# Optimization experiments

Hardware: AMD Instinct MI355X
Metric: run time of the kernel (lower is better)

## Reference

```python
import jax, jax.numpy as jnp
import numpy as np
from jax import lax

GAMMA = 2        # unused in forward (kept for fidelity to source)
PW = 10.0
THRESHOLD = 1.0
ERODE = 3
BACKZERO = 0

B, C, D, H, W = 2, 1, 128, 256, 256


def setup_inputs() -> dict:
    key = jax.random.key(0)
    k1, k2 = jax.random.split(key)
    inp = jax.random.normal(k1, (B, C, D, H, W), dtype=jnp.float32)
    tgt = jax.random.uniform(k2, (B, C, D, H, W), dtype=jnp.float32)
    return {"input": inp, "target": tgt}


def _box_sum_3d(x, r):
    # All-ones (2r+1)^3 conv3d with padding=r == sliding-window sum (shape-preserving).
    k = 2 * r + 1
    return lax.reduce_window(
        x, 0.0, lax.add,
        window_dimensions=(1, 1, k, k, k),
        window_strides=(1, 1, 1, 1, 1),
        padding=[(0, 0), (0, 0), (r, r), (r, r), (r, r)],
    )


def reference(input, target):
    # weight = clamp(target, 0, threshold); zero out voxels exactly at threshold
    w = jnp.clip(target, 0.0, THRESHOLD)
    w = w - THRESHOLD * (w == THRESHOLD).astype(jnp.float32)
    # box-filter "erosion" then binarize
    w = _box_sum_3d(w, ERODE)
    w = (w > 0).astype(jnp.float32)
    w = 1.0 + w * PW
    if BACKZERO != 0:
        mask = (input < 0).astype(jnp.float32) * (target == 0).astype(jnp.float32)
        w = w * (1.0 - mask)
    loss = jnp.abs(target - input) * w
    return jnp.mean(loss)
```

## Files before the change

### kernel.cpp

```cpp
#include <hip/hip_runtime.h>
#include <stdint.h>

#define BB 2
#define DD 128
#define HH 256
#define WW 256
static constexpr int64_t N = (int64_t)BB * DD * HH * WW;
static constexpr int WPR    = WW / 64;
static constexpr int NWORDS = BB * DD * HH * WPR;
static constexpr int NROWS  = BB * DD * HH;
static constexpr int K1_BLOCKS = NROWS / 8;
static constexpr int K2_BLOCKS = (HH / 16) * (DD / 16) * (BB * WPR);

__global__ __launch_bounds__(256) void mask_xdil_sum(const float* __restrict__ tgt,
                                                     const float* __restrict__ inp,
                                                     uint64_t* __restrict__ mask,
                                                     double* __restrict__ p0) {
    const int wave = threadIdx.x >> 6;
    const int lane = threadIdx.x & 63;
    float s = 0.0f;

    #pragma unroll
    for (int r = 0; r < 2; ++r) {
        const int row = blockIdx.x * 8 + wave * 2 + r;
        const int64_t base = (int64_t)row * WW;
        const float4 t = ((const float4*)(tgt + base))[lane];
        const float4 a = ((const float4*)(inp + base))[lane];

        s += fabsf(t.x - a.x) + fabsf(t.y - a.y)
           + fabsf(t.z - a.z) + fabsf(t.w - a.w);

        const uint64_t b0 = __ballot(t.x > 0.0f && t.x < 1.0f);
        const uint64_t b1 = __ballot(t.y > 0.0f && t.y < 1.0f);
        const uint64_t b2 = __ballot(t.z > 0.0f && t.z < 1.0f);
        const uint64_t b3 = __ballot(t.w > 0.0f && t.w < 1.0f);

        const uint64_t U  = b0 | b1 | b2 | b3;
        const uint64_t d0 = U | ((b1 | b2 | b3) << 1);
        const uint64_t d1 = U | ((b2 | b3) << 1) | (b0 >> 1);
        const uint64_t d2 = U | (b3 << 1) | ((b0 | b1) >> 1);
        const uint64_t d3 = U | ((b0 | b1 | b2) >> 1);

        const uint64_t dv = (lane & 2) ? ((lane & 1) ? d3 : d2)
                                       : ((lane & 1) ? d1 : d0);
        if (lane < 4)
            mask[(int64_t)row * WPR + lane] = dv;
    }

    #pragma unroll
    for (int off = 32; off > 0; off >>= 1)
        s += __shfl_down(s, off, 64);
    __shared__ float wsum[4];
    if (lane == 0) wsum[wave] = s;
    __syncthreads();
    if (threadIdx.x == 0)
        p0[blockIdx.x] = (double)((wsum[0] + wsum[1]) + (wsum[2] + wsum[3]));
}

__global__ __launch_bounds__(256) void yz_dil_reduce(const uint64_t* __restrict__ in,
                                                     const float* __restrict__ inp,
                                                     const float* __restrict__ tgt,
                                                     double* __restrict__ p1) {
    __shared__ uint64_t raw[22][23];
    __shared__ uint64_t yd[22][17];
    const int ty = threadIdx.x & 15;
    const int tz = threadIdx.x >> 4;
    const int y0 = blockIdx.x * 16;
    const int z0 = blockIdx.y * 16;
    const int b  = blockIdx.z >> 2;
    const int wx = blockIdx.z & 3;

    for (int idx = threadIdx.x; idx < 22 * 22; idx += 256) {
        const int zz = idx / 22, yy = idx % 22;
        const int gz = z0 - 3 + zz, gy = y0 - 3 + yy;
        uint64_t v = 0;
        if (gz >= 0 && gz < DD && gy >= 0 && gy < HH)
            v = in[(((int64_t)(b * DD + gz)) * HH + gy) * WPR + wx];
        raw[zz][yy] = v;
    }
    __syncthreads();

    for (int idx = threadIdx.x; idx < 22 * 16; idx += 256) {
        const int zz = idx >> 4, yy = idx & 15;
        uint64_t v = 0;
        #pragma unroll
        for (int d = 0; d < 7; d++) v |= raw[zz][yy + d];
        yd[zz][yy] = v;
    }
    __syncthreads();

    uint64_t v = 0;
    #pragma unroll
    for (int d = 0; d < 7; d++) v |= yd[tz + d][ty];

    float sab = 0.0f;
    if (v != ~0ull) {
        uint64_t z = ~v;
        const int64_t vox = (((int64_t)(b * DD + z0 + tz)) * HH + y0 + ty) * WW + wx;
        while (z) {
            const int l = __ffsll((unsigned long long)z) - 1;
            z &= z - 1;
            const int64_t o = vox + 4 * (int64_t)l;
            sab += fabsf(tgt[o] - inp[o]);
        }
    }

    #pragma unroll
    for (int off = 32; off > 0; off >>= 1)
        sab += __shfl_down(sab, off, 64);
    __shared__ float ws[4];
    const int lane = threadIdx.x & 63;
    const int wv   = threadIdx.x >> 6;
    if (lane == 0) ws[wv] = sab;
    __syncthreads();
    if (threadIdx.x == 0) {
        const int flat = blockIdx.x + gridDim.x * (blockIdx.y + gridDim.y * blockIdx.z);
        p1[flat] = (double)((ws[0] + ws[1]) + (ws[2] + ws[3]));
    }
}

__global__ __launch_bounds__(1024) void finalize(const double* __restrict__ p0,
                                                 const double* __restrict__ p1,
                                                 float* __restrict__ out) {
    double s0 = 0.0, sa = 0.0;
    for (int i = threadIdx.x; i < K1_BLOCKS; i += 1024) s0 += p0[i];
    for (int i = threadIdx.x; i < K2_BLOCKS; i += 1024) sa += p1[i];
    #pragma unroll
    for (int off = 32; off > 0; off >>= 1) {
        s0 += __shfl_down(s0, off, 64);
        sa += __shfl_down(sa, off, 64);
    }
    __shared__ double w0[16], wa[16];
    const int lane = threadIdx.x & 63;
    const int wv   = threadIdx.x >> 6;
    if (lane == 0) { w0[wv] = s0; wa[wv] = sa; }
    __syncthreads();
    if (threadIdx.x == 0) {
        double S0 = 0.0, SA = 0.0;
        #pragma unroll
        for (int k = 0; k < 16; k++) { S0 += w0[k]; SA += wa[k]; }
        out[0] = (float)((11.0 * S0 - 10.0 * SA) / (double)N);
    }
}

extern "C" void kernel_launch(void* const* d_in, const int* in_sizes, int n_in,
                              void* d_out, int out_size, void* d_ws, size_t ws_size,
                              hipStream_t stream) {
    const float* inp = (const float*)d_in[0];
    const float* tgt = (const float*)d_in[1];
    float* out = (float*)d_out;

    double*   p0    = (double*)d_ws;
    double*   p1    = (double*)((char*)d_ws + 96 * 1024);
    uint64_t* mask0 = (uint64_t*)((char*)d_ws + 256 * 1024);

    mask_xdil_sum<<<K1_BLOCKS, 256, 0, stream>>>(tgt, inp, mask0, p0);
    yz_dil_reduce<<<dim3(HH / 16, DD / 16, BB * WPR), 256, 0, stream>>>(mask0, inp, tgt, p1);
    finalize<<<1, 1024, 0, stream>>>(p0, p1, out);
}
```

Baseline: 149.4 us.

## Fuse final reduction into second kernel via atomics and batch row loads

The separate finalize launch is removed. Each block of the second kernel folds a slice of the first kernel's per-wave partials with its own partial sum, adds the result atomically to a global accumulator, and the last block (found with a ticket counter) writes the mean. The first kernel now uses a fixed grid of 2048 blocks. Each wave handles 8 strided rows and issues 4 rows of loads at a time to raise memory-level parallelism. This saves one launch and the tail reduction, at the cost of double atomics and a nondeterministic summation order.

Result: slower. 170.1 us (+13.9%).

```diff
diff --git a/kernel.cpp b/kernel.cpp
--- a/kernel.cpp
+++ b/kernel.cpp
@@ -7,60 +7,71 @@
 #define WW 256
 static constexpr int64_t N = (int64_t)BB * DD * HH * WW;
 static constexpr int WPR    = WW / 64;
-static constexpr int NWORDS = BB * DD * HH * WPR;
 static constexpr int NROWS  = BB * DD * HH;
-static constexpr int K1_BLOCKS = NROWS / 8;
+static constexpr int K1_BLOCKS = 2048;
+static constexpr int NWAVES = K1_BLOCKS * 4;
+static constexpr int ROWS_PER_WAVE = NROWS / NWAVES;
 static constexpr int K2_BLOCKS = (HH / 16) * (DD / 16) * (BB * WPR);
+static constexpr int P0_PER_K2 = NWAVES / K2_BLOCKS;
 
 __global__ __launch_bounds__(256) void mask_xdil_sum(const float* __restrict__ tgt,
                                                      const float* __restrict__ inp,
                                                      uint64_t* __restrict__ mask,
-                                                     double* __restrict__ p0) {
-    const int wave = threadIdx.x >> 6;
+                                                     double* __restrict__ p0,
+                                                     double* __restrict__ acc,
+                                                     unsigned* __restrict__ counter) {
     const int lane = threadIdx.x & 63;
+    const int wg   = (blockIdx.x << 2) | (threadIdx.x >> 6);
+
+    if (blockIdx.x == 0 && threadIdx.x == 0) { *acc = 0.0; *counter = 0u; }
+
     float s = 0.0f;
+    #pragma unroll
+    for (int h = 0; h < 2; ++h) {
+        float4 t[4], a[4];
+        #pragma unroll
+        for (int k = 0; k < 4; ++k) {
+            const int row = wg + (h * 4 + k) * NWAVES;
+            t[k] = ((const float4*)(tgt + (int64_t)row * WW))[lane];
+            a[k] = ((const float4*)(inp + (int64_t)row * WW))[lane];
+        }
+        #pragma unroll
+        for (int k = 0; k < 4; ++k) {
+            const int row = wg + (h * 4 + k) * NWAVES;
+            s += fabsf(t[k].x - a[k].x) + fabsf(t[k].y - a[k].y)
+               + fabsf(t[k].z - a[k].z) + fabsf(t[k].w - a[k].w);
 
-    #pragma unroll
-    for (int r = 0; r < 2; ++r) {
-        const int row = blockIdx.x * 8 + wave * 2 + r;
-        const int64_t base = (int64_t)row * WW;
-        const float4 t = ((const float4*)(tgt + base))[lane];
-        const float4 a = ((const float4*)(inp + base))[lane];
+            const uint64_t b0 = __ballot(t[k].x > 0.0f && t[k].x < 1.0f);
+            const uint64_t b1 = __ballot(t[k].y > 0.0f && t[k].y < 1.0f);
+            const uint64_t b2 = __ballot(t[k].z > 0.0f && t[k].z < 1.0f);
+            const uint64_t b3 = __ballot(t[k].w > 0.0f && t[k].w < 1.0f);
 
-        s += fabsf(t.x - a.x) + fabsf(t.y - a.y)
-           + fabsf(t.z - a.z) + fabsf(t.w - a.w);
+            const uint64_t U  = b0 | b1 | b2 | b3;
+            const uint64_t d0 = U | ((b1 | b2 | b3) << 1);
+            const uint64_t d1 = U | ((b2 | b3) << 1) | (b0 >> 1);
+            const uint64_t d2 = U | (b3 << 1) | ((b0 | b1) >> 1);
+            const uint64_t d3 = U | ((b0 | b1 | b2) >> 1);
 
-        const uint64_t b0 = __ballot(t.x > 0.0f && t.x < 1.0f);
-        const uint64_t b1 = __ballot(t.y > 0.0f && t.y < 1.0f);
-        const uint64_t b2 = __ballot(t.z > 0.0f && t.z < 1.0f);
-        const uint64_t b3 = __ballot(t.w > 0.0f && t.w < 1.0f);
-
-        const uint64_t U  = b0 | b1 | b2 | b3;
-        const uint64_t d0 = U | ((b1 | b2 | b3) << 1);
-        const uint64_t d1 = U | ((b2 | b3) << 1) | (b0 >> 1);
-        const uint64_t d2 = U | (b3 << 1) | ((b0 | b1) >> 1);
-        const uint64_t d3 = U | ((b0 | b1 | b2) >> 1);
-
-        const uint64_t dv = (lane & 2) ? ((lane & 1) ? d3 : d2)
-                                       : ((lane & 1) ? d1 : d0);
-        if (lane < 4)
-            mask[(int64_t)row * WPR + lane] = dv;
+            const uint64_t dv = (lane & 2) ? ((lane & 1) ? d3 : d2)
+                                           : ((lane & 1) ? d1 : d0);
+            if (lane < 4)
+                mask[(int64_t)row * WPR + lane] = dv;
+        }
     }
 
     #pragma unroll
     for (int off = 32; off > 0; off >>= 1)
         s += __shfl_down(s, off, 64);
-    __shared__ float wsum[4];
-    if (lane == 0) wsum[wave] = s;
-    __syncthreads();
-    if (threadIdx.x == 0)
-        p0[blockIdx.x] = (double)((wsum[0] + wsum[1]) + (wsum[2] + wsum[3]));
+    if (lane == 0) p0[wg] = (double)s;
 }
 
 __global__ __launch_bounds__(256) void yz_dil_reduce(const uint64_t* __restrict__ in,
                                                      const float* __restrict__ inp,
                                                      const float* __restrict__ tgt,
-                                                     double* __restrict__ p1) {
+                                                     const double* __restrict__ p0,
+                                                     double* __restrict__ acc,
+                                                     unsigned* __restrict__ counter,
+                                                     float* __restrict__ out) {
     __shared__ uint64_t raw[22][23];
     __shared__ uint64_t yd[22][17];
     const int ty = threadIdx.x & 15;
@@ -113,33 +124,20 @@
     const int wv   = threadIdx.x >> 6;
     if (lane == 0) ws[wv] = sab;
     __syncthreads();
+
     if (threadIdx.x == 0) {
         const int flat = blockIdx.x + gridDim.x * (blockIdx.y + gridDim.y * blockIdx.z);
-        p1[flat] = (double)((ws[0] + ws[1]) + (ws[2] + ws[3]));
-    }
-}
-
-__global__ __launch_bounds__(1024) void finalize(const double* __restrict__ p0,
-                                                 const double* __restrict__ p1,
-                                                 float* __restrict__ out) {
-    double s0 = 0.0, sa = 0.0;
-    for (int i = threadIdx.x; i < K1_BLOCKS; i += 1024) s0 += p0[i];
-    for (int i = threadIdx.x; i < K2_BLOCKS; i += 1024) sa += p1[i];
-    #pragma unroll
-    for (int off = 32; off > 0; off >>= 1) {
-        s0 += __shfl_down(s0, off, 64);
-        sa += __shfl_down(sa, off, 64);
-    }
-    __shared__ double w0[16], wa[16];
-    const int lane = threadIdx.x & 63;
-    const int wv   = threadIdx.x >> 6;
-    if (lane == 0) { w0[wv] = s0; wa[wv] = sa; }
-    __syncthreads();
-    if (threadIdx.x == 0) {
-        double S0 = 0.0, SA = 0.0;
+        double s0 = 0.0;
         #pragma unroll
-        for (int k = 0; k < 16; k++) { S0 += w0[k]; SA += wa[k]; }
-        out[0] = (float)((11.0 * S0 - 10.0 * SA) / (double)N);
+        for (int k = 0; k < P0_PER_K2; ++k) s0 += p0[flat * P0_PER_K2 + k];
+        const double sa = (double)((ws[0] + ws[1]) + (ws[2] + ws[3]));
+        atomicAdd(acc, 11.0 * s0 - 10.0 * sa);
+        __threadfence();
+        const unsigned ticket = atomicAdd(counter, 1u);
+        if (ticket == (unsigned)(K2_BLOCKS - 1)) {
+            const double total = atomicAdd(acc, 0.0);
+            out[0] = (float)(total / (double)N);
+        }
     }
 }
 
@@ -150,11 +148,12 @@
     const float* tgt = (const float*)d_in[1];
     float* out = (float*)d_out;
 
-    double*   p0    = (double*)d_ws;
-    double*   p1    = (double*)((char*)d_ws + 96 * 1024);
-    uint64_t* mask0 = (uint64_t*)((char*)d_ws + 256 * 1024);
+    double*   p0      = (double*)d_ws;
+    double*   acc     = (double*)((char*)d_ws + 96 * 1024);
+    unsigned* counter = (unsigned*)((char*)d_ws + 96 * 1024 + 64);
+    uint64_t* mask0   = (uint64_t*)((char*)d_ws + 256 * 1024);
 
-    mask_xdil_sum<<<K1_BLOCKS, 256, 0, stream>>>(tgt, inp, mask0, p0);
-    yz_dil_reduce<<<dim3(HH / 16, DD / 16, BB * WPR), 256, 0, stream>>>(mask0, inp, tgt, p1);
-    finalize<<<1, 1024, 0, stream>>>(p0, p1, out);
+    mask_xdil_sum<<<K1_BLOCKS, 256, 0, stream>>>(tgt, inp, mask0, p0, acc, counter);
+    yz_dil_reduce<<<dim3(HH / 16, DD / 16, BB * WPR), 256, 0, stream>>>(
+        mask0, inp, tgt, p0, acc, counter, out);
 }
```

## Fold finalize into second kernel via last-block atomic reduction

Applied to the files above, without the earlier changes.

Removes the separate single-block finalize launch. The second kernel now folds the per-row partial sums from the first kernel into its per-block contribution and uses an atomic ticket counter so the last block does the final reduction. The first kernel now handles one row per wave, launches twice as many blocks, and writes per-row float partials without a shared-memory block reduction. This saves a kernel launch and a serial tail, at the cost of atomics and a counter reset at the start of the first kernel.

Measured after the change: 173.4 us. 16.1% more time.

```diff
diff --git a/kernel.cpp b/kernel.cpp
--- a/kernel.cpp
+++ b/kernel.cpp
@@ -7,60 +7,58 @@
 #define WW 256
 static constexpr int64_t N = (int64_t)BB * DD * HH * WW;
 static constexpr int WPR    = WW / 64;
-static constexpr int NWORDS = BB * DD * HH * WPR;
 static constexpr int NROWS  = BB * DD * HH;
-static constexpr int K1_BLOCKS = NROWS / 8;
+static constexpr int K1_BLOCKS = NROWS / 4;
 static constexpr int K2_BLOCKS = (HH / 16) * (DD / 16) * (BB * WPR);
+static constexpr int ROWS_PER_K2 = NROWS / K2_BLOCKS;
 
 __global__ __launch_bounds__(256) void mask_xdil_sum(const float* __restrict__ tgt,
                                                      const float* __restrict__ inp,
                                                      uint64_t* __restrict__ mask,
-                                                     double* __restrict__ p0) {
+                                                     float* __restrict__ p0f,
+                                                     unsigned* __restrict__ counter) {
     const int wave = threadIdx.x >> 6;
     const int lane = threadIdx.x & 63;
-    float s = 0.0f;
+    const int row  = blockIdx.x * 4 + wave;
 
-    #pragma unroll
-    for (int r = 0; r < 2; ++r) {
-        const int row = blockIdx.x * 8 + wave * 2 + r;
-        const int64_t base = (int64_t)row * WW;
-        const float4 t = ((const float4*)(tgt + base))[lane];
-        const float4 a = ((const float4*)(inp + base))[lane];
+    if (blockIdx.x == 0 && threadIdx.x == 0) *counter = 0u;
 
-        s += fabsf(t.x - a.x) + fabsf(t.y - a.y)
-           + fabsf(t.z - a.z) + fabsf(t.w - a.w);
+    const int64_t base = (int64_t)row * WW;
+    const float4 t = ((const float4*)(tgt + base))[lane];
+    const float4 a = ((const float4*)(inp + base))[lane];
 
-        const uint64_t b0 = __ballot(t.x > 0.0f && t.x < 1.0f);
-        const uint64_t b1 = __ballot(t.y > 0.0f && t.y < 1.0f);
-        const uint64_t b2 = __ballot(t.z > 0.0f && t.z < 1.0f);
-        const uint64_t b3 = __ballot(t.w > 0.0f && t.w < 1.0f);
+    float s = fabsf(t.x - a.x) + fabsf(t.y - a.y)
+            + fabsf(t.z - a.z) + fabsf(t.w - a.w);
 
-        const uint64_t U  = b0 | b1 | b2 | b3;
-        const uint64_t d0 = U | ((b1 | b2 | b3) << 1);
-        const uint64_t d1 = U | ((b2 | b3) << 1) | (b0 >> 1);
-        const uint64_t d2 = U | (b3 << 1) | ((b0 | b1) >> 1);
-        const uint64_t d3 = U | ((b0 | b1 | b2) >> 1);
+    const uint64_t b0 = __ballot(t.x > 0.0f && t.x < 1.0f);
+    const uint64_t b1 = __ballot(t.y > 0.0f && t.y < 1.0f);
+    const uint64_t b2 = __ballot(t.z > 0.0f && t.z < 1.0f);
+    const uint64_t b3 = __ballot(t.w > 0.0f && t.w < 1.0f);
 
-        const uint64_t dv = (lane & 2) ? ((lane & 1) ? d3 : d2)
-                                       : ((lane & 1) ? d1 : d0);
-        if (lane < 4)
-            mask[(int64_t)row * WPR + lane] = dv;
-    }
+    const uint64_t U  = b0 | b1 | b2 | b3;
+    const uint64_t d0 = U | ((b1 | b2 | b3) << 1);
+    const uint64_t d1 = U | ((b2 | b3) << 1) | (b0 >> 1);
+    const uint64_t d2 = U | (b3 << 1) | ((b0 | b1) >> 1);
+    const uint64_t d3 = U | ((b0 | b1 | b2) >> 1);
+
+    const uint64_t dv = (lane & 2) ? ((lane & 1) ? d3 : d2)
+                                   : ((lane & 1) ? d1 : d0);
+    if (lane < 4)
+        mask[(int64_t)row * WPR + lane] = dv;
 
     #pragma unroll
     for (int off = 32; off > 0; off >>= 1)
         s += __shfl_down(s, off, 64);
-    __shared__ float wsum[4];
-    if (lane == 0) wsum[wave] = s;
-    __syncthreads();
-    if (threadIdx.x == 0)
-        p0[blockIdx.x] = (double)((wsum[0] + wsum[1]) + (wsum[2] + wsum[3]));
+    if (lane == 0) p0f[row] = s;
 }
 
 __global__ __launch_bounds__(256) void yz_dil_reduce(const uint64_t* __restrict__ in,
                                                      const float* __restrict__ inp,
                                                      const float* __restrict__ tgt,
-                                                     double* __restrict__ p1) {
+                                                     const float* __restrict__ p0f,
+                                                     double* __restrict__ p1,
+                                                     unsigned* __restrict__ counter,
+                                                     float* __restrict__ out) {
     __shared__ uint64_t raw[22][23];
     __shared__ uint64_t yd[22][17];
     const int ty = threadIdx.x & 15;
@@ -69,6 +67,9 @@
     const int z0 = blockIdx.y * 16;
     const int b  = blockIdx.z >> 2;
     const int wx = blockIdx.z & 3;
+    const int lane = threadIdx.x & 63;
+    const int wv   = threadIdx.x >> 6;
+    const int flat = blockIdx.x + gridDim.x * (blockIdx.y + gridDim.y * blockIdx.z);
 
     for (int idx = threadIdx.x; idx < 22 * 22; idx += 256) {
         const int zz = idx / 22, yy = idx % 22;
@@ -109,37 +110,43 @@
     for (int off = 32; off > 0; off >>= 1)
         sab += __shfl_down(sab, off, 64);
     __shared__ float ws[4];
-    const int lane = threadIdx.x & 63;
-    const int wv   = threadIdx.x >> 6;
+    __shared__ int lastflag;
     if (lane == 0) ws[wv] = sab;
     __syncthreads();
-    if (threadIdx.x == 0) {
-        const int flat = blockIdx.x + gridDim.x * (blockIdx.y + gridDim.y * blockIdx.z);
-        p1[flat] = (double)((ws[0] + ws[1]) + (ws[2] + ws[3]));
+
+    if (wv == 0) {
+        double s0 = (double)p0f[flat * ROWS_PER_K2 + lane];
+        #pragma unroll
+        for (int off = 32; off > 0; off >>= 1)
+            s0 += __shfl_down(s0, off, 64);
+        int lf = 0;
+        if (lane == 0) {
+            const double sa = (double)((ws[0] + ws[1]) + (ws[2] + ws[3]));
+            const double contrib = 11.0 * s0 - 10.0 * sa;
+            __hip_atomic_store(&p1[flat], contrib, __ATOMIC_RELEASE,
+                               __HIP_MEMORY_SCOPE_AGENT);
+            const unsigned tk = __hip_atomic_fetch_add(counter, 1u, __ATOMIC_ACQ_REL,
+                                                       __HIP_MEMORY_SCOPE_AGENT);
+            lf = (tk == (unsigned)(K2_BLOCKS - 1)) ? 1 : 0;
+        }
+        if (threadIdx.x == 0) lastflag = lf;
     }
-}
+    __syncthreads();
 
-__global__ __launch_bounds__(1024) void finalize(const double* __restrict__ p0,
-                                                 const double* __restrict__ p1,
-                                                 float* __restrict__ out) {
-    double s0 = 0.0, sa = 0.0;
-    for (int i = threadIdx.x; i < K1_BLOCKS; i += 1024) s0 += p0[i];
-    for (int i = threadIdx.x; i < K2_BLOCKS; i += 1024) sa += p1[i];
-    #pragma unroll
-    for (int off = 32; off > 0; off >>= 1) {
-        s0 += __shfl_down(s0, off, 64);
-        sa += __shfl_down(sa, off, 64);
-    }
-    __shared__ double w0[16], wa[16];
-    const int lane = threadIdx.x & 63;
-    const int wv   = threadIdx.x >> 6;
-    if (lane == 0) { w0[wv] = s0; wa[wv] = sa; }
-    __syncthreads();
-    if (threadIdx.x == 0) {
-        double S0 = 0.0, SA = 0.0;
+    if (lastflag) {
+        __threadfence();
+        double acc = 0.0;
+        for (int i = threadIdx.x; i < K2_BLOCKS; i += 256)
+            acc += __hip_atomic_load(&p1[i], __ATOMIC_RELAXED,
+                                     __HIP_MEMORY_SCOPE_AGENT);
         #pragma unroll
-        for (int k = 0; k < 16; k++) { S0 += w0[k]; SA += wa[k]; }
-        out[0] = (float)((11.0 * S0 - 10.0 * SA) / (double)N);
+        for (int off = 32; off > 0; off >>= 1)
+            acc += __shfl_down(acc, off, 64);
+        __shared__ double wd[4];
+        if (lane == 0) wd[wv] = acc;
+        __syncthreads();
+        if (threadIdx.x == 0)
+            out[0] = (float)(((wd[0] + wd[1]) + (wd[2] + wd[3])) / (double)N);
     }
 }
 
@@ -150,11 +157,12 @@
     const float* tgt = (const float*)d_in[1];
     float* out = (float*)d_out;
 
-    double*   p0    = (double*)d_ws;
-    double*   p1    = (double*)((char*)d_ws + 96 * 1024);
-    uint64_t* mask0 = (uint64_t*)((char*)d_ws + 256 * 1024);
+    float*    p0f     = (float*)d_ws;
+    double*   p1      = (double*)((char*)d_ws + 256 * 1024);
+    unsigned* counter = (unsigned*)((char*)d_ws + 272 * 1024);
+    uint64_t* mask0   = (uint64_t*)((char*)d_ws + 512 * 1024);
 
-    mask_xdil_sum<<<K1_BLOCKS, 256, 0, stream>>>(tgt, inp, mask0, p0);
-    yz_dil_reduce<<<dim3(HH / 16, DD / 16, BB * WPR), 256, 0, stream>>>(mask0, inp, tgt, p1);
-    finalize<<<1, 1024, 0, stream>>>(p0, p1, out);
+    mask_xdil_sum<<<K1_BLOCKS, 256, 0, stream>>>(tgt, inp, mask0, p0f, counter);
+    yz_dil_reduce<<<dim3(HH / 16, DD / 16, BB * WPR), 256, 0, stream>>>(
+        mask0, inp, tgt, p0f, p1, counter, out);
 }
```
